# Optimization experiments

Hardware: AMD Instinct MI355X
Metric: run time of the kernel (lower is better)

The kernel has to match this reference:

```python
import jax, jax.numpy as jnp
import numpy as np

B, D, HID, DC, K = 32768, 64, 512, 128, 12
CLAMP = 1.0
L1 = D // 2          # GLOW split lengths
L2 = D - L1
INIT = 0.01          # torch code rescales all params to 0.01*randn


def setup_inputs() -> dict:
    key = jax.random.key(0)
    ks = iter(jax.random.split(key, 16))
    # FrEIA PermuteRandom: np.random.seed(k); np.random.permutation(D)
    perms = jnp.asarray(
        np.stack([np.random.RandomState(k).permutation(D) for k in range(K)]),
        dtype=jnp.int32)
    f32 = jnp.float32
    return {
        'q_feat': jax.random.normal(next(ks), (B, 1, D), f32),
        'H': jax.random.normal(next(ks), (B, DC), f32),
        'perms': perms,
        'an_logscale': INIT * jax.random.normal(next(ks), (K, D), f32),
        'an_bias': INIT * jax.random.normal(next(ks), (K, D), f32),
        's1_W1': INIT * jax.random.normal(next(ks), (K, HID, L1 + DC), f32),
        's1_b1': INIT * jax.random.normal(next(ks), (K, HID), f32),
        's1_W2': INIT * jax.random.normal(next(ks), (K, 2 * L2, HID), f32),
        's1_b2': INIT * jax.random.normal(next(ks), (K, 2 * L2), f32),
        's2_W1': INIT * jax.random.normal(next(ks), (K, HID, L2 + DC), f32),
        's2_b1': INIT * jax.random.normal(next(ks), (K, HID), f32),
        's2_W2': INIT * jax.random.normal(next(ks), (K, 2 * L1, HID), f32),
        's2_b2': INIT * jax.random.normal(next(ks), (K, 2 * L1), f32),
    }


def _mlp(x, W1, b1, W2, b2):
    # torch Linear: y = x @ W.T + b
    h = jax.nn.relu(x @ W1.T + b1)
    return h @ W2.T + b2


def _log_e(s):
    # FrEIA GLOW soft clamp: log e(s) = clamp * 0.636 * atan(s / clamp)
    return CLAMP * 0.636 * jnp.arctan(s / CLAMP)


def reference(q_feat, H, perms, an_logscale, an_bias,
              s1_W1, s1_b1, s1_W2, s1_b2,
              s2_W1, s2_b1, s2_W2, s2_b2):
    x = q_feat.reshape(q_feat.shape[0], -1)          # Flatten: (B,1,D)->(B,D)
    logj = jnp.zeros(x.shape[0], x.dtype)

    def block(carry, p):
        x, logj = carry
        perm, ls, bi, w11, b11, w12, b12, w21, b21, w22, b22 = p
        x = x[:, perm]                               # PermuteRandom (logdet 0)
        x = x * jnp.exp(ls) + bi                     # ActNorm
        logj = logj + jnp.sum(ls)
        x1, x2 = x[:, :L1], x[:, L1:]                # GLOW coupling
        r2 = _mlp(jnp.concatenate([x2, H], 1), w21, b21, w22, b22)
        le2 = _log_e(r2[:, :L1])
        y1 = jnp.exp(le2) * x1 + r2[:, L1:]
        r1 = _mlp(jnp.concatenate([y1, H], 1), w11, b11, w12, b12)
        le1 = _log_e(r1[:, :L2])
        y2 = jnp.exp(le1) * x2 + r1[:, L2:]
        logj = logj + jnp.sum(le1, axis=1) + jnp.sum(le2, axis=1)
        return (jnp.concatenate([y1, y2], 1), logj), None

    (z, logj), _ = jax.lax.scan(
        block, (x, logj),
        (perms, an_logscale, an_bias,
         s1_W1, s1_b1, s1_W2, s1_b2,
         s2_W1, s2_b1, s2_W2, s2_b2))
    return z, logj
```

## Files before the change

### kernel.cpp

```cpp
#include <hip/hip_runtime.h>
#include <hip/hip_bf16.h>
#include <math.h>

#define B_ROWS 32768

typedef __attribute__((ext_vector_type(8)))  short        s8v;
typedef __attribute__((ext_vector_type(4)))  float        f4v;
typedef __attribute__((ext_vector_type(2)))  unsigned int u2v;
typedef __attribute__((ext_vector_type(4)))  unsigned int u4v;

__device__ __forceinline__ short f2bf(float f){
  unsigned u = __builtin_bit_cast(unsigned, f);
  u = (u + 0x7fffu + ((u >> 16) & 1u)) >> 16;
  return (short)u;
}

#define MFMA16(A,B,C) __builtin_amdgcn_mfma_f32_16x16x32_bf16((A),(B),(C),0,0,0)

#define OXFT 0
#define XFT_S 132
#define OHB  33792
#define HB_S 136
#define RB_S 68
#define OW1  68608
#define W1BUF 43008
#define W1_S 168
#define OB1  154624
#define OB2  158720
#define OLJ  159232
#define OPERM 159744
#define OELS 160000
#define OBIV 160256
#define OSLS 160512
#define SM_SZ 160528

#define O_S1W1 0
#define O_S1W2 983040
#define O_S2W1 1376256
#define O_S2W2 2359296
#define W_TOTAL 2752512

__global__ void cvtw(const float* __restrict__ s1w1, const float* __restrict__ s1w2,
                     const float* __restrict__ s2w1, const float* __restrict__ s2w2,
                     unsigned short* __restrict__ dst)
{
  long t = (long)blockIdx.x * blockDim.x + threadIdx.x;
  if (t >= W_TOTAL) return;
  float v;
  if      (t < O_S1W2) v = s1w1[t];
  else if (t < O_S2W1) v = s1w2[t - O_S1W2];
  else if (t < O_S2W2) v = s2w1[t - O_S2W1];
  else                 v = s2w2[t - O_S2W2];
  dst[t] = (unsigned short)f2bf(v);
}

template<int USEBF>
__device__ __forceinline__ s8v ldw(const unsigned short* wb, const float* wf, int off){
  if (USEBF){
    return *(const s8v*)(wb + off);
  } else {
    f4v a = *(const f4v*)(wf + off);
    f4v b = *(const f4v*)(wf + off + 4);
    s8v r;
    r[0]=f2bf(a[0]); r[1]=f2bf(a[1]); r[2]=f2bf(a[2]); r[3]=f2bf(a[3]);
    r[4]=f2bf(b[0]); r[5]=f2bf(b[1]); r[6]=f2bf(b[2]); r[7]=f2bf(b[3]);
    return r;
  }
}

struct MP { const unsigned short* w1b; const float* w1f;
            const unsigned short* w2b; const float* w2f;
            const float* b1; const float* b2; };

__device__ __forceinline__ MP getmp(int m, const unsigned short* wbf,
    const float* s1W1f, const float* s1W2f, const float* s2W1f, const float* s2W2f,
    const float* s1b1, const float* s1b2, const float* s2b1, const float* s2b2)
{
  int blk = m >> 1;
  MP r;
  if (m & 1){
    r.w1b = wbf + O_S1W1 + (size_t)blk*81920; r.w1f = s1W1f + (size_t)blk*81920;
    r.w2b = wbf + O_S1W2 + (size_t)blk*32768; r.w2f = s1W2f + (size_t)blk*32768;
    r.b1 = s1b1 + blk*512; r.b2 = s1b2 + blk*64;
  } else {
    r.w1b = wbf + O_S2W1 + (size_t)blk*81920; r.w1f = s2W1f + (size_t)blk*81920;
    r.w2b = wbf + O_S2W2 + (size_t)blk*32768; r.w2f = s2W2f + (size_t)blk*32768;
    r.b1 = s2b1 + blk*512; r.b2 = s2b2 + blk*64;
  }
  return r;
}

template<int USEBF>
__device__ __forceinline__ void issue_w1(const MP& p, int cchunk, int tid,
                                         u4v wt[5], f4v wtf[10])
{
  if (USEBF){
    const unsigned short* s = p.w1b + cchunk*20480;
    #pragma unroll
    for (int k = 0; k < 5; ++k) wt[k] = *(const u4v*)(s + (size_t)(k*512+tid)*8);
  } else {
    const float* s = p.w1f + cchunk*20480;
    #pragma unroll
    for (int k = 0; k < 10; ++k) wtf[k] = *(const f4v*)(s + (size_t)(k*512+tid)*4);
  }
}

template<int USEBF>
__device__ __forceinline__ void write_w1(char* sm, int buf, int tid,
                                         const u4v wt[5], const f4v wtf[10])
{
  short* W1n = (short*)(sm + OW1 + buf*W1BUF);
  if (USEBF){
    #pragma unroll
    for (int k = 0; k < 5; ++k){
      int i = k*512 + tid, row = i/20, c16 = i - row*20;
      *(u4v*)(W1n + row*W1_S + c16*8) = wt[k];
    }
  } else {
    #pragma unroll
    for (int k = 0; k < 10; ++k){
      int i = k*512 + tid, row = i/40, c4 = i - row*40;
      f4v v = wtf[k];
      unsigned u0 = (unsigned)(unsigned short)f2bf(v[0]) | ((unsigned)(unsigned short)f2bf(v[1])<<16);
      unsigned u1 = (unsigned)(unsigned short)f2bf(v[2]) | ((unsigned)(unsigned short)f2bf(v[3])<<16);
      *(u2v*)(W1n + row*W1_S + c4*4) = (u2v){u0,u1};
    }
  }
}

template<int USEBF>
__device__ __forceinline__ void load_w2(const MP& p, int c, int hw, int l15, int lq, s8v w2o[4]){
  #pragma unroll
  for (int kk = 0; kk < 4; ++kk)
    w2o[kk] = ldw<USEBF>(p.w2b, p.w2f, (hw*16 + l15)*512 + c*128 + kk*32 + lq*8);
}

template<int USEBF>
__device__ __forceinline__ void mlp_body(char* sm, int tid, int m,
    const MP& cur, const MP& nxt, const s8v hfr[4][4], s8v w2cur[4])
{
  const int lane = tid & 63, wave = tid >> 6;
  const int hw = wave >> 1, ng = wave & 1;
  const int l15 = lane & 15, lq = lane >> 4;
  const int bp = m & 1;
  float* XFT = (float*)(sm + OXFT);
  short* HB  = (short*)(sm + OHB);
  float* RB  = (float*)(sm + OHB);
  float* B1L = (float*)(sm + OB1);
  float* B2L = (float*)(sm + OB2);
  float* LOGJ= (float*)(sm + OLJ);

  const int xbase = bp ? 0 : 32;
  s8v xk[4];
  #pragma unroll
  for (int nt = 0; nt < 4; ++nt){
    int b = ng*64 + nt*16 + l15;
    s8v v;
    #pragma unroll
    for (int i = 0; i < 8; ++i)
      v[i] = f2bf(XFT[(xbase + lq*8 + i)*XFT_S + b]);
    xk[nt] = v;
  }

  f4v racc[4];
  { f4v bv = *(const f4v*)(B2L + bp*64 + hw*16 + lq*4);
    #pragma unroll
    for (int nt = 0; nt < 4; ++nt) racc[nt] = bv; }

  #pragma unroll
  for (int c = 0; c < 4; ++c){
    u4v wt[5]; f4v wtf[10];
    s8v w2n[4];
    const MP& pn = (c < 3) ? cur : nxt;
    const int cn = (c < 3) ? c + 1 : 0;
    issue_w1<USEBF>(pn, cn, tid, wt, wtf);
    load_w2<USEBF>(pn, cn, hw, l15, lq, w2n);
    float b1t = 0.f, b2t = 0.f;
    if (c == 3){
      b1t = nxt.b1[tid];
      if (tid < 64) b2t = nxt.b2[tid];
    }

    const short* W1c = (const short*)(sm + OW1 + (c&1)*W1BUF);
    f4v acc[2][4];
    #pragma unroll
    for (int mt = 0; mt < 2; ++mt){
      f4v bv = *(const f4v*)(B1L + bp*512 + c*128 + hw*32 + mt*16 + lq*4);
      #pragma unroll
      for (int nt = 0; nt < 4; ++nt) acc[mt][nt] = bv;
    }
    #pragma unroll
    for (int kk = 0; kk < 5; ++kk){
      s8v a0 = *(const s8v*)(W1c + (hw*32 +  0 + l15)*W1_S + kk*32 + lq*8);
      s8v a1 = *(const s8v*)(W1c + (hw*32 + 16 + l15)*W1_S + kk*32 + lq*8);
      #pragma unroll
      for (int nt = 0; nt < 4; ++nt){
        s8v bb = (kk == 0) ? xk[nt] : hfr[nt][kk-1];
        acc[0][nt] = MFMA16(a0, bb, acc[0][nt]);
        acc[1][nt] = MFMA16(a1, bb, acc[1][nt]);
      }
    }
    #pragma unroll
    for (int mt = 0; mt < 2; ++mt)
      #pragma unroll
      for (int nt = 0; nt < 4; ++nt){
        float h0 = fmaxf(acc[mt][nt][0],0.f), h1 = fmaxf(acc[mt][nt][1],0.f);
        float h2 = fmaxf(acc[mt][nt][2],0.f), h3 = fmaxf(acc[mt][nt][3],0.f);
        unsigned u0 = (unsigned)(unsigned short)f2bf(h0) | ((unsigned)(unsigned short)f2bf(h1)<<16);
        unsigned u1 = (unsigned)(unsigned short)f2bf(h2) | ((unsigned)(unsigned short)f2bf(h3)<<16);
        *(u2v*)(HB + (ng*64 + nt*16 + l15)*HB_S + hw*32 + mt*16 + lq*4) = (u2v){u0,u1};
      }
    write_w1<USEBF>(sm, cn & 1, tid, wt, wtf);
    if (c == 3){
      B1L[(bp^1)*512 + tid] = b1t;
      if (tid < 64) B2L[(bp^1)*64 + tid] = b2t;
    }
    __syncthreads();

    #pragma unroll
    for (int kk = 0; kk < 4; ++kk){
      s8v aw = w2cur[kk];
      #pragma unroll
      for (int nt = 0; nt < 4; ++nt){
        s8v bb = *(const s8v*)(HB + (ng*64 + nt*16 + l15)*HB_S + kk*32 + lq*8);
        racc[nt] = MFMA16(aw, bb, racc[nt]);
      }
    }
    #pragma unroll
    for (int kk = 0; kk < 4; ++kk) w2cur[kk] = w2n[kk];
    __syncthreads();
  }

  #pragma unroll
  for (int nt = 0; nt < 4; ++nt)
    *(f4v*)(RB + (ng*64 + nt*16 + l15)*RB_S + hw*16 + lq*4) = racc[nt];
  __syncthreads();

  {
    int b = tid & 127, og = tid >> 7;
    f4v L0 = *(const f4v*)(RB + b*RB_S + og*8);
    f4v L1 = *(const f4v*)(RB + b*RB_S + og*8 + 4);
    f4v R0 = *(const f4v*)(RB + b*RB_S + 32 + og*8);
    f4v R1 = *(const f4v*)(RB + b*RB_S + 32 + og*8 + 4);
    float le[8] = {L0[0],L0[1],L0[2],L0[3],L1[0],L1[1],L1[2],L1[3]};
    float ra[8] = {R0[0],R0[1],R0[2],R0[3],R1[0],R1[1],R1[2],R1[3]};
    float part = 0.f;
    #pragma unroll
    for (int j = 0; j < 8; ++j){
      float l = 0.636f * atanf(le[j]);
      int d = bp*32 + og*8 + j;
      float y = __expf(l) * XFT[d*XFT_S + b] + ra[j];
      XFT[d*XFT_S + b] = y;
      part += l;
    }
    atomicAdd(&LOGJ[b], part);
  }
  __syncthreads();
}

template<int USEBF>
__global__ __launch_bounds__(512, 2) void cinn_t(
    const float* __restrict__ q, const float* __restrict__ Hg,
    const int* __restrict__ perms,
    const float* __restrict__ ls_g, const float* __restrict__ bi_g,
    const float* __restrict__ s1b1, const float* __restrict__ s1b2,
    const float* __restrict__ s2b1, const float* __restrict__ s2b2,
    const unsigned short* __restrict__ wbf,
    const float* __restrict__ s1W1f, const float* __restrict__ s1W2f,
    const float* __restrict__ s2W1f, const float* __restrict__ s2W2f,
    float* __restrict__ outz, float* __restrict__ outlj)
{
  __shared__ __align__(16) char sm[SM_SZ];
  const int tid = threadIdx.x;
  const int rowbase = blockIdx.x * 128;
  const int lane = tid & 63, wave = tid >> 6;
  const int hw = wave >> 1, ng = wave & 1;
  const int l15 = lane & 15, lq = lane >> 4;

  float* XFT = (float*)(sm + OXFT);
  float* B1L = (float*)(sm + OB1);
  float* B2L = (float*)(sm + OB2);
  float* LOGJ = (float*)(sm + OLJ);
  int*   PERM = (int*)(sm + OPERM);
  float* ELS  = (float*)(sm + OELS);
  float* BIV  = (float*)(sm + OBIV);
  float* SLSp = (float*)(sm + OSLS);

  {
    int b = tid >> 2, j = tid & 3;
    const float* src = q + (size_t)(rowbase + b)*64 + j*16;
    #pragma unroll
    for (int i = 0; i < 4; ++i){
      f4v v = *(const f4v*)(src + 4*i);
      #pragma unroll
      for (int jj = 0; jj < 4; ++jj)
        XFT[(j*16 + 4*i + jj)*XFT_S + b] = v[jj];
    }
  }
  if (tid < 128) LOGJ[tid] = 0.f;
  if (tid == 0)  *SLSp = 0.f;
  __syncthreads();
  if (tid < 64){
    float p = 0.f;
    #pragma unroll
    for (int k = 0; k < 12; ++k) p += ls_g[k*64 + tid];
    atomicAdd(SLSp, p);
  }

  s8v hfr[4][4];
  #pragma unroll
  for (int nt = 0; nt < 4; ++nt){
    int b = rowbase + ng*64 + nt*16 + l15;
    #pragma unroll
    for (int kkh = 0; kkh < 4; ++kkh){
      const float* hp = Hg + (size_t)b*128 + kkh*32 + lq*8;
      f4v a = *(const f4v*)hp;
      f4v c = *(const f4v*)(hp + 4);
      s8v r;
      r[0]=f2bf(a[0]); r[1]=f2bf(a[1]); r[2]=f2bf(a[2]); r[3]=f2bf(a[3]);
      r[4]=f2bf(c[0]); r[5]=f2bf(c[1]); r[6]=f2bf(c[2]); r[7]=f2bf(c[3]);
      hfr[nt][kkh] = r;
    }
  }

  s8v w2cur[4];
  {
    MP p0 = getmp(0, wbf, s1W1f, s1W2f, s2W1f, s2W2f, s1b1, s1b2, s2b1, s2b2);
    u4v wt[5]; f4v wtf[10];
    issue_w1<USEBF>(p0, 0, tid, wt, wtf);
    write_w1<USEBF>(sm, 0, tid, wt, wtf);
    B1L[tid] = p0.b1[tid];
    if (tid < 64) B2L[tid] = p0.b2[tid];
    load_w2<USEBF>(p0, 0, hw, l15, lq, w2cur);
  }

  for (int m = 0; m < 24; ++m){
    if (!(m & 1)){
      int blk = m >> 1;
      if (tid < 64){
        PERM[tid] = perms[blk*64 + tid];
        ELS[tid]  = __expf(ls_g[blk*64 + tid]);
        BIV[tid]  = bi_g[blk*64 + tid];
      }
      __syncthreads();
      {
        int d = lane, bg = wave;
        int pd = PERM[d];
        f4v v[4];
        #pragma unroll
        for (int i = 0; i < 4; ++i)
          v[i] = *(const f4v*)(XFT + pd*XFT_S + bg*16 + 4*i);
        __syncthreads();
        float e = ELS[d], bi = BIV[d];
        #pragma unroll
        for (int i = 0; i < 4; ++i){
          #pragma unroll
          for (int jj = 0; jj < 4; ++jj) v[i][jj] = fmaf(v[i][jj], e, bi);
          *(f4v*)(XFT + d*XFT_S + bg*16 + 4*i) = v[i];
        }
      }
      __syncthreads();
    }
    MP cur = getmp(m, wbf, s1W1f, s1W2f, s2W1f, s2W2f, s1b1, s1b2, s2b1, s2b2);
    MP nxt = getmp(m < 23 ? m + 1 : 23, wbf, s1W1f, s1W2f, s2W1f, s2W2f, s1b1, s1b2, s2b1, s2b2);
    mlp_body<USEBF>(sm, tid, m, cur, nxt, hfr, w2cur);
  }

  {
    int b = tid >> 2, j = tid & 3;
    float* dst = outz + (size_t)(rowbase + b)*64 + j*16;
    #pragma unroll
    for (int i = 0; i < 4; ++i){
      f4v w;
      #pragma unroll
      for (int jj = 0; jj < 4; ++jj)
        w[jj] = XFT[(j*16 + 4*i + jj)*XFT_S + b];
      *(f4v*)(dst + 4*i) = w;
    }
  }
  if (tid < 128) outlj[rowbase + tid] = LOGJ[tid] + *SLSp;
}

extern "C" void kernel_launch(void* const* d_in, const int* in_sizes, int n_in,
                              void* d_out, int out_size, void* d_ws, size_t ws_size,
                              hipStream_t stream)
{
  const float* q    = (const float*)d_in[0];
  const float* Hg   = (const float*)d_in[1];
  const int*   perms= (const int*)  d_in[2];
  const float* ls   = (const float*)d_in[3];
  const float* bi   = (const float*)d_in[4];
  const float* s1W1 = (const float*)d_in[5];
  const float* s1b1 = (const float*)d_in[6];
  const float* s1W2 = (const float*)d_in[7];
  const float* s1b2 = (const float*)d_in[8];
  const float* s2W1 = (const float*)d_in[9];
  const float* s2b1 = (const float*)d_in[10];
  const float* s2W2 = (const float*)d_in[11];
  const float* s2b2 = (const float*)d_in[12];
  float* outz  = (float*)d_out;
  float* outlj = outz + (size_t)B_ROWS * 64;

  int usebf = (ws_size >= (size_t)W_TOTAL * 2) ? 1 : 0;
  unsigned short* wbf = (unsigned short*)d_ws;
  if (usebf){
    cvtw<<<2688, 1024, 0, stream>>>(s1W1, s1W2, s2W1, s2W2, wbf);
    cinn_t<1><<<256, 512, 0, stream>>>(q, Hg, perms, ls, bi,
                                       s1b1, s1b2, s2b1, s2b2,
                                       wbf, s1W1, s1W2, s2W1, s2W2,
                                       outz, outlj);
  } else {
    cinn_t<0><<<256, 512, 0, stream>>>(q, Hg, perms, ls, bi,
                                       s1b1, s1b2, s2b1, s2b2,
                                       wbf, s1W1, s1W2, s2W1, s2W2,
                                       outz, outlj);
  }
}
```

Baseline: 299.7 us.

## Split second MLP layer over hidden-dim chunks per wave, removing per-chunk barrier

Each wave now computes a partial sum of the second-layer output over its own 32-wide slice of the hidden dimension. It reads back only the HB columns it just wrote, so the second __syncthreads per chunk can be dropped. The four per-wave partial outputs are stored as bf16 in spare LDS slots and summed during the coupling epilogue. In exchange there are more accumulator registers (16 f4v instead of 4), extra reduction loads, and a precision loss from rounding the partials to bf16 before summing, with the risk that the spare LDS slots overlap live data.

```diff
diff --git a/kernel.cpp b/kernel.cpp
--- a/kernel.cpp
+++ b/kernel.cpp
@@ -14,6 +14,11 @@
   u = (u + 0x7fffu + ((u >> 16) & 1u)) >> 16;
   return (short)u;
 }
+__device__ __forceinline__ unsigned pk2(float a, float b){
+  return (unsigned)(unsigned short)f2bf(a) | ((unsigned)(unsigned short)f2bf(b) << 16);
+}
+__device__ __forceinline__ float bf_lo(unsigned u){ return __builtin_bit_cast(float, u << 16); }
+__device__ __forceinline__ float bf_hi(unsigned u){ return __builtin_bit_cast(float, u & 0xffff0000u); }
 
 #define MFMA16(A,B,C) __builtin_amdgcn_mfma_f32_16x16x32_bf16((A),(B),(C),0,0,0)
 
@@ -21,7 +26,6 @@
 #define XFT_S 132
 #define OHB  33792
 #define HB_S 136
-#define RB_S 68
 #define OW1  68608
 #define W1BUF 43008
 #define W1_S 168
@@ -34,6 +38,9 @@
 #define OSLS 160512
 #define SM_SZ 160528
 
+#define SL_S 68
+#define SLOT_B 17408
+
 #define O_S1W1 0
 #define O_S1W2 983040
 #define O_S2W1 1376256
@@ -121,9 +128,7 @@
     for (int k = 0; k < 10; ++k){
       int i = k*512 + tid, row = i/40, c4 = i - row*40;
       f4v v = wtf[k];
-      unsigned u0 = (unsigned)(unsigned short)f2bf(v[0]) | ((unsigned)(unsigned short)f2bf(v[1])<<16);
-      unsigned u1 = (unsigned)(unsigned short)f2bf(v[2]) | ((unsigned)(unsigned short)f2bf(v[3])<<16);
-      *(u2v*)(W1n + row*W1_S + c4*4) = (u2v){u0,u1};
+      *(u2v*)(W1n + row*W1_S + c4*4) = (u2v){pk2(v[0],v[1]), pk2(v[2],v[3])};
     }
   }
 }
@@ -131,8 +136,8 @@
 template<int USEBF>
 __device__ __forceinline__ void load_w2(const MP& p, int c, int hw, int l15, int lq, s8v w2o[4]){
   #pragma unroll
-  for (int kk = 0; kk < 4; ++kk)
-    w2o[kk] = ldw<USEBF>(p.w2b, p.w2f, (hw*16 + l15)*512 + c*128 + kk*32 + lq*8);
+  for (int ot = 0; ot < 4; ++ot)
+    w2o[ot] = ldw<USEBF>(p.w2b, p.w2f, (ot*16 + l15)*512 + c*128 + hw*32 + lq*8);
 }
 
 template<int USEBF>
@@ -145,7 +150,6 @@
   const int bp = m & 1;
   float* XFT = (float*)(sm + OXFT);
   short* HB  = (short*)(sm + OHB);
-  float* RB  = (float*)(sm + OHB);
   float* B1L = (float*)(sm + OB1);
   float* B2L = (float*)(sm + OB2);
   float* LOGJ= (float*)(sm + OLJ);
@@ -162,19 +166,21 @@
     xk[nt] = v;
   }
 
-  f4v racc[4];
-  { f4v bv = *(const f4v*)(B2L + bp*64 + hw*16 + lq*4);
-    #pragma unroll
-    for (int nt = 0; nt < 4; ++nt) racc[nt] = bv; }
+  f4v racc[4][4];
+  #pragma unroll
+  for (int ot = 0; ot < 4; ++ot){
+    f4v bv = (f4v){0.f,0.f,0.f,0.f};
+    if (hw == 0) bv = *(const f4v*)(B2L + bp*64 + ot*16 + lq*4);
+    #pragma unroll
+    for (int nt = 0; nt < 4; ++nt) racc[ot][nt] = bv;
+  }
 
   #pragma unroll
   for (int c = 0; c < 4; ++c){
     u4v wt[5]; f4v wtf[10];
-    s8v w2n[4];
     const MP& pn = (c < 3) ? cur : nxt;
     const int cn = (c < 3) ? c + 1 : 0;
     issue_w1<USEBF>(pn, cn, tid, wt, wtf);
-    load_w2<USEBF>(pn, cn, hw, l15, lq, w2n);
     float b1t = 0.f, b2t = 0.f;
     if (c == 3){
       b1t = nxt.b1[tid];
@@ -206,44 +212,52 @@
       for (int nt = 0; nt < 4; ++nt){
         float h0 = fmaxf(acc[mt][nt][0],0.f), h1 = fmaxf(acc[mt][nt][1],0.f);
         float h2 = fmaxf(acc[mt][nt][2],0.f), h3 = fmaxf(acc[mt][nt][3],0.f);
-        unsigned u0 = (unsigned)(unsigned short)f2bf(h0) | ((unsigned)(unsigned short)f2bf(h1)<<16);
-        unsigned u1 = (unsigned)(unsigned short)f2bf(h2) | ((unsigned)(unsigned short)f2bf(h3)<<16);
-        *(u2v*)(HB + (ng*64 + nt*16 + l15)*HB_S + hw*32 + mt*16 + lq*4) = (u2v){u0,u1};
+        *(u2v*)(HB + (ng*64 + nt*16 + l15)*HB_S + hw*32 + mt*16 + lq*4) = (u2v){pk2(h0,h1), pk2(h2,h3)};
       }
+    #pragma unroll
+    for (int nt = 0; nt < 4; ++nt){
+      s8v bb = *(const s8v*)(HB + (ng*64 + nt*16 + l15)*HB_S + hw*32 + lq*8);
+      #pragma unroll
+      for (int ot = 0; ot < 4; ++ot)
+        racc[ot][nt] = MFMA16(w2cur[ot], bb, racc[ot][nt]);
+    }
     write_w1<USEBF>(sm, cn & 1, tid, wt, wtf);
     if (c == 3){
       B1L[(bp^1)*512 + tid] = b1t;
       if (tid < 64) B2L[(bp^1)*64 + tid] = b2t;
     }
+    load_w2<USEBF>(pn, cn, hw, l15, lq, w2cur);
     __syncthreads();
-
-    #pragma unroll
-    for (int kk = 0; kk < 4; ++kk){
-      s8v aw = w2cur[kk];
-      #pragma unroll
-      for (int nt = 0; nt < 4; ++nt){
-        s8v bb = *(const s8v*)(HB + (ng*64 + nt*16 + l15)*HB_S + kk*32 + lq*8);
-        racc[nt] = MFMA16(aw, bb, racc[nt]);
-      }
-    }
-    #pragma unroll
-    for (int kk = 0; kk < 4; ++kk) w2cur[kk] = w2n[kk];
-    __syncthreads();
-  }
-
-  #pragma unroll
-  for (int nt = 0; nt < 4; ++nt)
-    *(f4v*)(RB + (ng*64 + nt*16 + l15)*RB_S + hw*16 + lq*4) = racc[nt];
+  }
+
+  {
+    short* SL = (hw < 2) ? (short*)(sm + OW1 + W1BUF + hw*SLOT_B)
+                         : (short*)(sm + OHB + (hw-2)*SLOT_B);
+    #pragma unroll
+    for (int ot = 0; ot < 4; ++ot)
+      #pragma unroll
+      for (int nt = 0; nt < 4; ++nt)
+        *(u2v*)(SL + (ng*64 + nt*16 + l15)*SL_S + ot*16 + lq*4) =
+          (u2v){pk2(racc[ot][nt][0], racc[ot][nt][1]), pk2(racc[ot][nt][2], racc[ot][nt][3])};
+  }
   __syncthreads();
 
   {
     int b = tid & 127, og = tid >> 7;
-    f4v L0 = *(const f4v*)(RB + b*RB_S + og*8);
-    f4v L1 = *(const f4v*)(RB + b*RB_S + og*8 + 4);
-    f4v R0 = *(const f4v*)(RB + b*RB_S + 32 + og*8);
-    f4v R1 = *(const f4v*)(RB + b*RB_S + 32 + og*8 + 4);
-    float le[8] = {L0[0],L0[1],L0[2],L0[3],L1[0],L1[1],L1[2],L1[3]};
-    float ra[8] = {R0[0],R0[1],R0[2],R0[3],R1[0],R1[1],R1[2],R1[3]};
+    float le[8] = {0,0,0,0,0,0,0,0}, ra[8] = {0,0,0,0,0,0,0,0};
+    #pragma unroll
+    for (int mslot = 0; mslot < 4; ++mslot){
+      const short* SL = (mslot < 2) ? (const short*)(sm + OW1 + W1BUF + mslot*SLOT_B)
+                                    : (const short*)(sm + OHB + (mslot-2)*SLOT_B);
+      u2v L0 = *(const u2v*)(SL + b*SL_S + og*8);
+      u2v L1 = *(const u2v*)(SL + b*SL_S + og*8 + 4);
+      u2v R0 = *(const u2v*)(SL + b*SL_S + 32 + og*8);
+      u2v R1 = *(const u2v*)(SL + b*SL_S + 32 + og*8 + 4);
+      le[0]+=bf_lo(L0[0]); le[1]+=bf_hi(L0[0]); le[2]+=bf_lo(L0[1]); le[3]+=bf_hi(L0[1]);
+      le[4]+=bf_lo(L1[0]); le[5]+=bf_hi(L1[0]); le[6]+=bf_lo(L1[1]); le[7]+=bf_hi(L1[1]);
+      ra[0]+=bf_lo(R0[0]); ra[1]+=bf_hi(R0[0]); ra[2]+=bf_lo(R0[1]); ra[3]+=bf_hi(R0[1]);
+      ra[4]+=bf_lo(R1[0]); ra[5]+=bf_hi(R1[0]); ra[6]+=bf_lo(R1[1]); ra[7]+=bf_hi(R1[1]);
+    }
     float part = 0.f;
     #pragma unroll
     for (int j = 0; j < 8; ++j){
```

Result: no change. 299.2 us (-0.2%).
